# Kernel optimization log

Measured on AMD Instinct MI355X. Metric: run time of the kernel, lower is better.

Reference implementation:

```python
import jax, jax.numpy as jnp
import numpy as np

EPS = 1e-7
KERNELS = ((5, 5), (7, 1), (1, 7))
SCALES = (60, 30, 15, 8)


def avg_pool(x, kh, kw):
    # PyTorch AvgPool2d(kernel, stride=1, padding=(kh//2, kw//2)), count_include_pad=True
    s = jax.lax.reduce_window(x, 0.0, jax.lax.add, (1, 1, kh, kw), (1, 1, 1, 1),
                              ((0, 0), (0, 0), (kh // 2, kh // 2), (kw // 2, kw // 2)))
    return s / (kh * kw)


def resize_bilinear(x, oh, ow):
    # F.interpolate(mode='bilinear', align_corners=True), NCHW
    B, C, H, W = x.shape
    def coords(o, s):
        pos = jnp.arange(o) * ((s - 1) / max(o - 1, 1))
        i0 = jnp.floor(pos).astype(jnp.int32)
        i1 = jnp.minimum(i0 + 1, s - 1)
        w = (pos - i0).astype(x.dtype)
        return w, i0, i1
    wy, y0, y1 = coords(oh, H)
    wx, x0, x1 = coords(ow, W)
    rows = x[:, :, y0, :] * (1 - wy)[None, None, :, None] + x[:, :, y1, :] * wy[None, None, :, None]
    return rows[:, :, :, x0] * (1 - wx) + rows[:, :, :, x1] * wx


def setup_inputs() -> dict:
    key = jax.random.key(0)
    ks = jax.random.split(key, 12)
    B, C, H, shot = 2, 1024, 60, 1
    hid, tdim = 256, 300
    return {
        "weight": jax.random.uniform(ks[0], (B, shot, 1, 1), dtype=jnp.float32),
        "query_feat_4": jax.random.normal(ks[1], (B, C, H, H), dtype=jnp.float32),
        "supp_feats": jax.random.normal(ks[2], (shot, B, C, H, H), dtype=jnp.float32),
        "masks": jax.random.uniform(ks[3], (shot, B, 1, 473, 473), dtype=jnp.float32),
        "k": jax.random.normal(ks[4], (B, hid, H, H), dtype=jnp.float32),
        "text": jax.random.normal(ks[5], (B, tdim), dtype=jnp.float32),
        "prototype": jax.random.normal(ks[6], (B, hid, 1, 1), dtype=jnp.float32),
        "w_q": jax.random.normal(ks[7], (tdim + hid, hid), dtype=jnp.float32) * 0.05,
        "w_k": jax.random.normal(ks[8], (hid, hid), dtype=jnp.float32) * 0.05,
        "w_bl": jax.random.normal(ks[9], (hid, hid), dtype=jnp.float32) * 0.05,
        "w_proj": jax.random.normal(ks[10], (hid, hid), dtype=jnp.float32) * 0.05,
        "b_proj": jnp.zeros((hid,), dtype=jnp.float32),
    }


def reference(weight, query_feat_4, supp_feats, masks, k, text, prototype, w_q, w_k, w_bl, w_proj, b_proj):
    # ---------------- SPM: self-activation prior mask ----------------
    B, C, H, W = query_feat_4.shape
    S = H * W
    # pooled query features per kernel (shared across supports)
    q_pooled = []
    for (kh, kw) in KERNELS:
        tq = avg_pool(query_feat_4, kh, kw).reshape(B, C, S)
        tq_t = jnp.transpose(tq, (0, 2, 1))                    # [B,S,C]
        qn = jnp.sqrt((tq_t ** 2).sum(-1, keepdims=True))      # [B,S,1]
        q_pooled.append((tq_t, qn))

    corr_list = []
    for i in range(supp_feats.shape[0]):  # loop over shot (small, fixed)
        tmp_mask = resize_bilinear(masks[i], H, W)
        s = supp_feats[i] * tmp_mask
        region = []
        for (kh, kw), (tq_t, qn) in zip(KERNELS, q_pooled):
            ts = avg_pool(s, kh, kw).reshape(B, C, S)          # [B,C,S]
            sn = jnp.sqrt((ts ** 2).sum(1, keepdims=True))     # [B,1,S]
            sim = jnp.matmul(tq_t, ts) / (jnp.matmul(qn, sn) + EPS) * qn  # [B,S,S]
            sim = sim.mean(2)                                  # [B,S]
            mn = sim.min(1, keepdims=True)
            mx = sim.max(1, keepdims=True)
            sim = (sim - mn) / (mx - mn + EPS)
            region.append(sim.reshape(B, H, W))
        corr_list.append(jnp.stack(region, 1).mean(1))         # [B,H,W]
    corr = jnp.stack(corr_list, 1)                             # [B,shot,H,W]
    corr1 = (weight * corr).sum(1, keepdims=True)              # [B,1,H,W]
    corr2 = resize_bilinear(corr1, SCALES[1], SCALES[1])
    corr3 = resize_bilinear(corr1, SCALES[2], SCALES[2])
    corr4 = resize_bilinear(corr1, SCALES[3], SCALES[3])

    # ---------------- APA: bi-linear cross-modal attention ----------------
    Bk, hid, h, w = k.shape
    proto = prototype.reshape(Bk, 1, hid)                      # [B,1,hid]
    q = jnp.concatenate([text[:, None, :], proto], axis=-1)    # [B,1,embed]
    kx = jnp.einsum('oi,bihw->bohw', w_k, k).reshape(Bk, hid, h * w)
    kx = jnp.transpose(kx, (0, 2, 1))                          # [B,S,hid]
    qx = jnp.einsum('bqe,eh->bqh', q, w_q)                     # [B,1,hid]
    qw = jnp.einsum('bqh,hd->bqd', qx, w_bl)                   # bi_linear score
    score = jnp.einsum('bqd,bsd->bqs', qw, kx)                 # [B,1,S]
    score = jax.nn.softmax(score, axis=-1)
    out = jnp.einsum('bqs,bsd->bqd', score, kx)
    out = jnp.einsum('bqd,do->bqo', out, w_proj) + b_proj      # proj (dropout=eval no-op)
    out = out + proto
    return corr1, corr2, corr3, corr4, out
```

## Files before the change

kernel.cpp:

```cpp
#include <hip/hip_runtime.h>
#include <math.h>

#define EPSF 1e-7f
#define Bsz 2
#define Cch 1024
#define Hh 60
#define Ssz 3600
#define HID 256
#define TDIM 300
#define MH 473

#define TROWS 15
#define LROWS 21
#define LPITCH 68
#define CPG 8

#define OFF_SN2   7200
#define OFF_DOT   28800
#define OFF_ACC   50400
#define OFF_SCORE 57600
#define OFF_WMAP  64800
#define OFF_V     86400
#define OFF_U     92544
#define OFF_KBAR  93056
#define ZERO_OFF  OFF_SN2
#define ZERO_CNT  (OFF_WMAP - OFF_SN2)

__global__ void __launch_bounds__(256) k_pool_sn2(const float* __restrict__ supp,
                                                  const float* __restrict__ masks,
                                                  float* __restrict__ sn2g) {
    __shared__ float  mk[LROWS * LPITCH];
    __shared__ float2 raw[LROWS * LPITCH];
    __shared__ float2 h5s[LROWS * LPITCH];
    __shared__ float2 h7s[LROWS * LPITCH];
    int tid = threadIdx.x;
    int tile = blockIdx.x;
    int cg = blockIdx.y;
    int b = blockIdx.z;
    int y0 = tile * TROWS;

    const float2 z2 = {0.f, 0.f};
    for (int i = tid; i < LROWS * LPITCH; i += 256) {
        mk[i] = 0.f; raw[i] = z2; h5s[i] = z2; h7s[i] = z2;
    }
    __syncthreads();

    int lr[5], lx[5]; bool lv[5], la[5];
    #pragma unroll
    for (int j = 0; j < 5; ++j) {
        int idx = tid + 256 * j;
        int r = idx / 60, x = idx - 60 * r;
        lr[j] = r; lx[j] = x;
        la[j] = idx < 1260;
        int iy = y0 - 3 + r;
        lv[j] = la[j] && (iy >= 0) && (iy < Hh);
    }
    #pragma unroll
    for (int j = 0; j < 5; ++j)
        if (lv[j]) {
            int iy = y0 - 3 + lr[j];
            mk[lr[j] * LPITCH + 4 + lx[j]] =
                masks[(size_t)b * MH * MH + (size_t)(iy * 8) * MH + lx[j] * 8];
        }

    int orow[4], ox[4]; bool ov[4];
    #pragma unroll
    for (int j = 0; j < 4; ++j) {
        int o = tid + 256 * j;
        int oy = o / 60, x = o - 60 * oy;
        orow[j] = oy + 3; ox[j] = x; ov[j] = o < 900;
    }
    float a0[4] = {0,0,0,0}, a1[4] = {0,0,0,0}, a2[4] = {0,0,0,0};

    const float* chbase = supp + ((size_t)b * Cch + (size_t)cg * CPG) * Ssz + (y0 - 3) * 60;
    float pf0[5], pf1[5];
    #pragma unroll
    for (int j = 0; j < 5; ++j) {
        pf0[j] = lv[j] ? chbase[tid + 256 * j] : 0.f;
        pf1[j] = lv[j] ? chbase[Ssz + tid + 256 * j] : 0.f;
    }

    for (int p = 0; p < CPG / 2; ++p) {
        __syncthreads();
        #pragma unroll
        for (int j = 0; j < 5; ++j)
            if (lv[j]) {
                float m = mk[lr[j] * LPITCH + 4 + lx[j]];
                raw[lr[j] * LPITCH + 4 + lx[j]] = make_float2(pf0[j] * m, pf1[j] * m);
            }
        __syncthreads();
        #pragma unroll
        for (int j = 0; j < 5; ++j)
            if (la[j]) {
                int base = lr[j] * LPITCH + 4 + lx[j];
                float2 m3 = raw[base - 3], m2 = raw[base - 2], m1 = raw[base - 1];
                float2 c0 = raw[base], p1 = raw[base + 1], p2 = raw[base + 2], p3 = raw[base + 3];
                float2 h5, h7;
                h5.x = m2.x + m1.x + c0.x + p1.x + p2.x;
                h5.y = m2.y + m1.y + c0.y + p1.y + p2.y;
                h7.x = h5.x + m3.x + p3.x;
                h7.y = h5.y + m3.y + p3.y;
                h5s[base] = h5; h7s[base] = h7;
            }
        __syncthreads();
        if (p + 1 < CPG / 2) {
            const float* nb = chbase + (size_t)(2 * p + 2) * Ssz;
            #pragma unroll
            for (int j = 0; j < 5; ++j) {
                pf0[j] = lv[j] ? nb[tid + 256 * j] : 0.f;
                pf1[j] = lv[j] ? nb[Ssz + tid + 256 * j] : 0.f;
            }
        }
        #pragma unroll
        for (int j = 0; j < 4; ++j)
            if (ov[j]) {
                int base = orow[j] * LPITCH + 4 + ox[j];
                float2 sa = h5s[base - 2*LPITCH], sb = h5s[base - LPITCH], sc0 = h5s[base];
                float2 sd = h5s[base + LPITCH], se = h5s[base + 2*LPITCH];
                float p55x = (sa.x + sb.x + sc0.x + sd.x + se.x) * (1.f / 25.f);
                float p55y = (sa.y + sb.y + sc0.y + sd.y + se.y) * (1.f / 25.f);
                float2 ra = raw[base - 3*LPITCH], rb = raw[base - 2*LPITCH], rc = raw[base - LPITCH];
                float2 rd = raw[base], re = raw[base + LPITCH], rf = raw[base + 2*LPITCH], rg = raw[base + 3*LPITCH];
                float p71x = (ra.x + rb.x + rc.x + rd.x + re.x + rf.x + rg.x) * (1.f / 7.f);
                float p71y = (ra.y + rb.y + rc.y + rd.y + re.y + rf.y + rg.y) * (1.f / 7.f);
                float2 h7v = h7s[base];
                float p17x = h7v.x * (1.f / 7.f), p17y = h7v.y * (1.f / 7.f);
                a0[j] += p55x * p55x + p55y * p55y;
                a1[j] += p71x * p71x + p71y * p71y;
                a2[j] += p17x * p17x + p17y * p17y;
            }
    }
    float* g0 = sn2g + ((size_t)b * 3 + 0) * Ssz;
    float* g1 = sn2g + ((size_t)b * 3 + 1) * Ssz;
    float* g2 = sn2g + ((size_t)b * 3 + 2) * Ssz;
    #pragma unroll
    for (int j = 0; j < 4; ++j)
        if (ov[j]) {
            int q = (y0 + orow[j] - 3) * 60 + ox[j];
            atomicAdd(&g0[q], a0[j]);
            atomicAdd(&g1[q], a1[j]);
            atomicAdd(&g2[q], a2[j]);
        }
}

__global__ void k_wmap(const float* __restrict__ sn2g, float* __restrict__ wmapg) {
    __shared__ float inv[LROWS * LPITCH];
    int tile = blockIdx.x;
    int bk = blockIdx.y;
    int kt = bk % 3;
    int tid = threadIdx.x;
    int y0 = tile * TROWS;
    for (int i = tid; i < LROWS * LPITCH; i += 256) inv[i] = 0.f;
    __syncthreads();
    const float* sn2 = sn2g + (size_t)bk * Ssz;
    #pragma unroll
    for (int j = 0; j < 5; ++j) {
        int idx = tid + 256 * j;
        if (idx < 1260) {
            int r = idx / 60, x = idx - 60 * r;
            int iy = y0 - 3 + r;
            if (iy >= 0 && iy < Hh)
                inv[r * LPITCH + 4 + x] = 1.0f / sqrtf(fmaxf(sn2[iy * 60 + x], 1e-30f));
        }
    }
    __syncthreads();
    int kh = (kt == 0) ? 5 : (kt == 1) ? 7 : 1;
    int kw = (kt == 0) ? 5 : (kt == 2) ? 7 : 1;
    int rh = kh / 2, rw = kw / 2;
    float norm = 1.f / (float)(kh * kw);
    #pragma unroll
    for (int j = 0; j < 4; ++j) {
        int o = tid + 256 * j;
        if (o < 900) {
            int oy = o / 60, x = o - 60 * oy;
            int base = (oy + 3) * LPITCH + 4 + x;
            float s = 0.f;
            for (int dy = -rh; dy <= rh; ++dy)
                for (int dx = -rw; dx <= rw; ++dx)
                    s += inv[base + dy * LPITCH + dx];
            wmapg[(size_t)bk * Ssz + (y0 + oy) * 60 + x] = s * norm;
        }
    }
}

__global__ void k_v(const float* __restrict__ supp, const float* __restrict__ masks,
                    float* __restrict__ ws) {
    int c = blockIdx.x, b = blockIdx.y;
    int tid = threadIdx.x;
    const float* sp = supp + ((size_t)b * Cch + c) * Ssz;
    const float* mbase = masks + (size_t)b * MH * MH;
    const float* w0 = ws + OFF_WMAP + (size_t)(b * 3 + 0) * Ssz;
    const float* w1 = ws + OFF_WMAP + (size_t)(b * 3 + 1) * Ssz;
    const float* w2 = ws + OFF_WMAP + (size_t)(b * 3 + 2) * Ssz;
    float a0 = 0, a1 = 0, a2 = 0;
    for (int q = tid; q < Ssz; q += 256) {
        int y = q / Hh, x = q - y * Hh;
        float s = sp[q] * mbase[(size_t)(y * 8) * MH + x * 8];
        a0 += s * w0[q]; a1 += s * w1[q]; a2 += s * w2[q];
    }
    __shared__ float red[3][256];
    red[0][tid] = a0; red[1][tid] = a1; red[2][tid] = a2;
    __syncthreads();
    for (int off = 128; off > 0; off >>= 1) {
        if (tid < off) {
            red[0][tid] += red[0][tid + off];
            red[1][tid] += red[1][tid + off];
            red[2][tid] += red[2][tid + off];
        }
        __syncthreads();
    }
    if (tid == 0) {
        ws[OFF_V + (size_t)(b * 3 + 0) * Cch + c] = red[0][0];
        ws[OFF_V + (size_t)(b * 3 + 1) * Cch + c] = red[1][0];
        ws[OFF_V + (size_t)(b * 3 + 2) * Cch + c] = red[2][0];
    }
}

__global__ void k_dot(const float* __restrict__ query, float* __restrict__ ws) {
    int qt = blockIdx.x, cc = blockIdx.y, b = blockIdx.z;
    int q = qt * 256 + threadIdx.x;
    if (q >= Ssz) return;
    const float* v0 = ws + OFF_V + (size_t)(b * 3 + 0) * Cch;
    const float* v1 = ws + OFF_V + (size_t)(b * 3 + 1) * Cch;
    const float* v2 = ws + OFF_V + (size_t)(b * 3 + 2) * Cch;
    float a0 = 0, a1 = 0, a2 = 0;
    int c0 = cc * 64;
    for (int c = c0; c < c0 + 64; ++c) {
        float qv = query[((size_t)b * Cch + c) * Ssz + q];
        a0 += qv * v0[c]; a1 += qv * v1[c]; a2 += qv * v2[c];
    }
    atomicAdd(&ws[OFF_DOT + (size_t)(b * 3 + 0) * Ssz + q], a0);
    atomicAdd(&ws[OFF_DOT + (size_t)(b * 3 + 1) * Ssz + q], a1);
    atomicAdd(&ws[OFF_DOT + (size_t)(b * 3 + 2) * Ssz + q], a2);
}

__global__ void k_sim(float* __restrict__ ws) {
    __shared__ float dpad[66 * LPITCH];
    __shared__ float h5p[66 * LPITCH];
    __shared__ float h7p[66 * LPITCH];
    __shared__ float red[256];
    int bk = blockIdx.x; int b = bk / 3; int kt = bk % 3;
    int tid = threadIdx.x;
    const float* dg = ws + OFF_DOT + (size_t)bk * Ssz;
    for (int i = tid; i < 66 * LPITCH; i += 256) {
        int r = i / LPITCH, col = i - r * LPITCH;
        int y = r - 3, x = col - 4;
        dpad[i] = (y >= 0 && y < Hh && x >= 0 && x < Hh) ? dg[y * Hh + x] : 0.f;
    }
    __syncthreads();
    for (int idx = tid; idx < 66 * 60; idx += 256) {
        int r = idx / 60, x = idx - 60 * r;
        int base = r * LPITCH + 4 + x;
        float m3 = dpad[base - 3], m2 = dpad[base - 2], m1 = dpad[base - 1];
        float c0 = dpad[base], p1 = dpad[base + 1], p2 = dpad[base + 2], p3 = dpad[base + 3];
        float h5 = m2 + m1 + c0 + p1 + p2;
        h5p[base] = h5;
        h7p[base] = h5 + m3 + p3;
    }
    __syncthreads();
    float norm = ((kt == 0) ? (1.f / 25.f) : (1.f / 7.f)) * (1.f / (float)Ssz);
    float vals[15];
    float vmin = INFINITY, vmax = -INFINITY;
    #pragma unroll
    for (int j = 0; j < 15; ++j) {
        int q = tid + j * 256;
        if (q < Ssz) {
            int y = q / Hh, x = q - y * Hh;
            int base = (y + 3) * LPITCH + 4 + x;
            float s;
            if (kt == 0)
                s = h5p[base - 2*LPITCH] + h5p[base - LPITCH] + h5p[base]
                  + h5p[base + LPITCH] + h5p[base + 2*LPITCH];
            else if (kt == 1)
                s = dpad[base - 3*LPITCH] + dpad[base - 2*LPITCH] + dpad[base - LPITCH]
                  + dpad[base] + dpad[base + LPITCH] + dpad[base + 2*LPITCH] + dpad[base + 3*LPITCH];
            else
                s = h7p[base];
            float val = s * norm;
            vals[j] = val;
            vmin = fminf(vmin, val); vmax = fmaxf(vmax, val);
        }
    }
    red[tid] = vmin; __syncthreads();
    for (int off = 128; off > 0; off >>= 1) {
        if (tid < off) red[tid] = fminf(red[tid], red[tid + off]);
        __syncthreads();
    }
    float mn = red[0]; __syncthreads();
    red[tid] = vmax; __syncthreads();
    for (int off = 128; off > 0; off >>= 1) {
        if (tid < off) red[tid] = fmaxf(red[tid], red[tid + off]);
        __syncthreads();
    }
    float mx = red[0];
    float inv = 1.f / (mx - mn + EPSF);
    #pragma unroll
    for (int j = 0; j < 15; ++j) {
        int q = tid + j * 256;
        if (q < Ssz) atomicAdd(&ws[OFF_ACC + (size_t)b * Ssz + q], (vals[j] - mn) * inv);
    }
}

__global__ void k_final(const float* __restrict__ weight, const float* __restrict__ ws,
                        float* __restrict__ out) {
    int idx = blockIdx.x * 256 + threadIdx.x;
    if (idx < Bsz * Ssz) {
        int b = idx / Ssz, q = idx - b * Ssz;
        out[idx] = weight[b] * (1.f / 3.f) * ws[OFF_ACC + (size_t)b * Ssz + q];
        return;
    }
    int r = idx - Bsz * Ssz;
    int O, outbase;
    if (r < 1800)       { O = 30; outbase = 7200; }
    else if (r < 2250)  { O = 15; outbase = 9000; r -= 1800; }
    else if (r < 2378)  { O = 8;  outbase = 9450; r -= 2250; }
    else return;
    int n = O * O;
    int b = r / n, p = r - b * n;
    int y = p / O, x = p - y * O;
    float sc = (float)(Hh - 1) / (float)(O - 1);
    float py = y * sc, px = x * sc;
    int y0 = (int)floorf(py), x0 = (int)floorf(px);
    int y1 = min(y0 + 1, Hh - 1), x1 = min(x0 + 1, Hh - 1);
    float wy = py - y0, wx = px - x0;
    const float* src = ws + OFF_ACC + (size_t)b * Ssz;
    float v = src[y0 * Hh + x0] * (1.f - wy) * (1.f - wx)
            + src[y1 * Hh + x0] * wy * (1.f - wx)
            + src[y0 * Hh + x1] * (1.f - wy) * wx
            + src[y1 * Hh + x1] * wy * wx;
    out[outbase + r] = v * weight[b] * (1.f / 3.f);
}

__global__ void __launch_bounds__(1024, 1)
k_apa_u(const float* __restrict__ text, const float* __restrict__ proto,
        const float* __restrict__ w_q, const float* __restrict__ w_bl,
        const float* __restrict__ w_k, float* __restrict__ ws) {
    int b = blockIdx.x;
    int tid = threadIdx.x;
    int lane = tid & 63, w = tid >> 6;
    __shared__ float4 p4[16][64];
    __shared__ float qxs[256], qws[256];
    const float4* wq4 = (const float4*)w_q;
    const float4* wbl4 = (const float4*)w_bl;
    const float4* wk4 = (const float4*)w_k;

    float4 acc = {0.f, 0.f, 0.f, 0.f};
    #pragma unroll
    for (int j = 0; j < 35; ++j) {
        int e = w + 16 * j;
        if (e < TDIM + HID) {
            float x = (e < TDIM) ? text[b * TDIM + e] : proto[b * HID + e - TDIM];
            float4 f = wq4[(size_t)e * 64 + lane];
            acc.x += x * f.x; acc.y += x * f.y; acc.z += x * f.z; acc.w += x * f.w;
        }
    }
    p4[w][lane] = acc;
    __syncthreads();
    if (tid < 256) {
        const float* pf = (const float*)p4;
        float s = 0.f;
        #pragma unroll
        for (int ww = 0; ww < 16; ++ww) s += pf[ww * 256 + tid];
        qxs[tid] = s;
    }
    __syncthreads();

    acc.x = acc.y = acc.z = acc.w = 0.f;
    #pragma unroll
    for (int j = 0; j < 16; ++j) {
        int e = w + 16 * j;
        float x = qxs[e];
        float4 f = wbl4[(size_t)e * 64 + lane];
        acc.x += x * f.x; acc.y += x * f.y; acc.z += x * f.z; acc.w += x * f.w;
    }
    p4[w][lane] = acc;
    __syncthreads();
    if (tid < 256) {
        const float* pf = (const float*)p4;
        float s = 0.f;
        #pragma unroll
        for (int ww = 0; ww < 16; ++ww) s += pf[ww * 256 + tid];
        qws[tid] = s;
    }
    __syncthreads();

    acc.x = acc.y = acc.z = acc.w = 0.f;
    #pragma unroll
    for (int j = 0; j < 16; ++j) {
        int e = w + 16 * j;
        float x = qws[e];
        float4 f = wk4[(size_t)e * 64 + lane];
        acc.x += x * f.x; acc.y += x * f.y; acc.z += x * f.z; acc.w += x * f.w;
    }
    p4[w][lane] = acc;
    __syncthreads();
    if (tid < 256) {
        const float* pf = (const float*)p4;
        float s = 0.f;
        #pragma unroll
        for (int ww = 0; ww < 16; ++ww) s += pf[ww * 256 + tid];
        ws[OFF_U + b * HID + tid] = s;
    }
}

__global__ void k_score(const float* __restrict__ kin, float* __restrict__ ws) {
    int st = blockIdx.x, ic = blockIdx.y, b = blockIdx.z;
    int s = st * 256 + threadIdx.x;
    if (s >= Ssz) return;
    const float* u = ws + OFF_U + b * HID;
    float acc = 0.f;
    int i0 = ic * 64;
    for (int i = i0; i < i0 + 64; ++i)
        acc += u[i] * kin[((size_t)b * HID + i) * Ssz + s];
    atomicAdd(&ws[OFF_SCORE + (size_t)b * Ssz + s], acc);
}

__global__ void k_softmax(float* __restrict__ ws) {
    int b = blockIdx.x; int tid = threadIdx.x;
    __shared__ float red[256];
    float* sc = ws + OFF_SCORE + (size_t)b * Ssz;
    float vals[15];
    float mx = -INFINITY;
    for (int j = 0; j < 15; ++j) {
        int s = tid + j * 256;
        if (s < Ssz) { vals[j] = sc[s]; mx = fmaxf(mx, vals[j]); }
    }
    red[tid] = mx; __syncthreads();
    for (int off = 128; off > 0; off >>= 1) {
        if (tid < off) red[tid] = fmaxf(red[tid], red[tid + off]);
        __syncthreads();
    }
    mx = red[0]; __syncthreads();
    float sum = 0.f;
    for (int j = 0; j < 15; ++j) {
        int s = tid + j * 256;
        if (s < Ssz) { vals[j] = expf(vals[j] - mx); sum += vals[j]; }
    }
    red[tid] = sum; __syncthreads();
    for (int off = 128; off > 0; off >>= 1) {
        if (tid < off) red[tid] += red[tid + off];
        __syncthreads();
    }
    float inv = 1.f / red[0];
    for (int j = 0; j < 15; ++j) {
        int s = tid + j * 256;
        if (s < Ssz) sc[s] = vals[j] * inv;
    }
}

__global__ void k_kbar(const float* __restrict__ kin, float* __restrict__ ws) {
    int i = blockIdx.x, b = blockIdx.y;
    int tid = threadIdx.x;
    const float* p = ws + OFF_SCORE + (size_t)b * Ssz;
    const float* kr = kin + ((size_t)b * HID + i) * Ssz;
    float acc = 0.f;
    for (int s = tid; s < Ssz; s += 256) acc += p[s] * kr[s];
    __shared__ float red[256];
    red[tid] = acc; __syncthreads();
    for (int off = 128; off > 0; off >>= 1) {
        if (tid < off) red[tid] += red[tid + off];
        __syncthreads();
    }
    if (tid == 0) ws[OFF_KBAR + b * HID + i] = red[0];
}

__global__ void __launch_bounds__(1024, 1)
k_apa_out(const float* __restrict__ w_k, const float* __restrict__ w_proj,
          const float* __restrict__ b_proj, const float* __restrict__ proto,
          const float* __restrict__ ws, float* __restrict__ out) {
    int b = blockIdx.x;
    int tid = threadIdx.x;
    int lane = tid & 63, w = tid >> 6;
    __shared__ float4 kbs[64];
    __shared__ float o1s[256];
    __shared__ float4 p4[16][64];
    const float4* wk4 = (const float4*)w_k;
    const float4* wp4 = (const float4*)w_proj;

    if (tid < 64) kbs[tid] = ((const float4*)(ws + OFF_KBAR + b * HID))[tid];
    __syncthreads();

    float4 kb4 = kbs[lane];
    #pragma unroll
    for (int r = 0; r < 16; ++r) {
        int h = w + 16 * r;
        float4 f = wk4[(size_t)h * 64 + lane];
        float p = f.x * kb4.x + f.y * kb4.y + f.z * kb4.z + f.w * kb4.w;
        #pragma unroll
        for (int m = 32; m >= 1; m >>= 1) p += __shfl_xor(p, m, 64);
        if (lane == 0) o1s[h] = p;
    }
    __syncthreads();

    float4 acc = {0.f, 0.f, 0.f, 0.f};
    #pragma unroll
    for (int j = 0; j < 16; ++j) {
        int d = w + 16 * j;
        float x = o1s[d];
        float4 f = wp4[(size_t)d * 64 + lane];
        acc.x += x * f.x; acc.y += x * f.y; acc.z += x * f.z; acc.w += x * f.w;
    }
    p4[w][lane] = acc;
    __syncthreads();
    if (tid < 256) {
        const float* pf = (const float*)p4;
        float s = 0.f;
        #pragma unroll
        for (int ww = 0; ww < 16; ++ww) s += pf[ww * 256 + tid];
        out[9578 + b * HID + tid] = s + b_proj[tid] + proto[b * HID + tid];
    }
}

extern "C" void kernel_launch(void* const* d_in, const int* in_sizes, int n_in,
                              void* d_out, int out_size, void* d_ws, size_t ws_size,
                              hipStream_t stream) {
    const float* weight = (const float*)d_in[0];
    const float* query  = (const float*)d_in[1];
    const float* supp   = (const float*)d_in[2];
    const float* masks  = (const float*)d_in[3];
    const float* kin    = (const float*)d_in[4];
    const float* text   = (const float*)d_in[5];
    const float* proto  = (const float*)d_in[6];
    const float* w_q    = (const float*)d_in[7];
    const float* w_k    = (const float*)d_in[8];
    const float* w_bl   = (const float*)d_in[9];
    const float* w_proj = (const float*)d_in[10];
    const float* b_proj = (const float*)d_in[11];
    float* out = (float*)d_out;
    float* ws  = (float*)d_ws;

    hipMemsetAsync(ws + ZERO_OFF, 0, (size_t)ZERO_CNT * sizeof(float), stream);

    k_pool_sn2<<<dim3(4, Cch / CPG, Bsz), 256, 0, stream>>>(supp, masks, ws + OFF_SN2);
    k_wmap<<<dim3(4, 6), 256, 0, stream>>>(ws + OFF_SN2, ws + OFF_WMAP);
    k_v<<<dim3(Cch, Bsz), 256, 0, stream>>>(supp, masks, ws);
    k_dot<<<dim3(15, Cch / 64, Bsz), 256, 0, stream>>>(query, ws);
    k_sim<<<6, 256, 0, stream>>>(ws);
    k_final<<<(Bsz * Ssz + 2378 + 255) / 256, 256, 0, stream>>>(weight, ws, out);

    k_apa_u<<<Bsz, 1024, 0, stream>>>(text, proto, w_q, w_bl, w_k, ws);
    k_score<<<dim3(15, 4, Bsz), 256, 0, stream>>>(kin, ws);
    k_softmax<<<Bsz, 256, 0, stream>>>(ws);
    k_kbar<<<dim3(HID, Bsz), 256, 0, stream>>>(kin, ws);
    k_apa_out<<<Bsz, 1024, 0, stream>>>(w_k, w_proj, b_proj, proto, ws, out);
}
```

Before: 232.1 us.

## Fuse sim/final and softmax/kbar, fold mask into wmap, replace atomics with partials

Several kernels are merged: the final normalisation and bilinear resize move into k_sim, and the softmax is folded into k_kbar, which recomputes max and sum per block from partial scores. The mask multiply moves into k_wmap so k_v becomes a float4 dot product with wave-shuffle reductions. Atomic accumulation in k_dot and k_score is replaced by per-group partial buffers summed by the consumer, and the memset becomes a zeroing kernel that also clears the output. The intent is fewer launches, fewer atomics and less reduction overhead. In exchange k_kbar redoes the softmax reduction in each of its 512 blocks and k_sim runs on only 6 blocks.

```diff
diff --git a/kernel.cpp b/kernel.cpp
--- a/kernel.cpp
+++ b/kernel.cpp
@@ -15,16 +15,21 @@
 #define LPITCH 68
 #define CPG 8
 
-#define OFF_SN2   7200
-#define OFF_DOT   28800
-#define OFF_ACC   50400
-#define OFF_SCORE 57600
-#define OFF_WMAP  64800
-#define OFF_V     86400
-#define OFF_U     92544
-#define OFF_KBAR  93056
-#define ZERO_OFF  OFF_SN2
-#define ZERO_CNT  (OFF_WMAP - OFF_SN2)
+#define OFF_SN2    0
+#define OFF_WMAP   21600
+#define OFF_V      43200
+#define OFF_U      49344
+#define OFF_KBAR   49856
+#define OFF_DOTP   50368
+#define OFF_SCOREP 395968
+#define ZERO_WS    21600
+#define ZERO_OUT   9578
+
+__global__ void k_zero(float* __restrict__ ws, float* __restrict__ out) {
+    int i = blockIdx.x * 256 + threadIdx.x;
+    if (i < ZERO_WS) ws[i] = 0.f;
+    else if (i < ZERO_WS + ZERO_OUT) out[i - ZERO_WS] = 0.f;
+}
 
 __global__ void __launch_bounds__(256) k_pool_sn2(const float* __restrict__ supp,
                                                   const float* __restrict__ masks,
@@ -143,11 +148,12 @@
         }
 }
 
-__global__ void k_wmap(const float* __restrict__ sn2g, float* __restrict__ wmapg) {
+__global__ void k_wmap(const float* __restrict__ sn2g, const float* __restrict__ masks,
+                       float* __restrict__ wmapg) {
     __shared__ float inv[LROWS * LPITCH];
     int tile = blockIdx.x;
     int bk = blockIdx.y;
-    int kt = bk % 3;
+    int b = bk / 3, kt = bk % 3;
     int tid = threadIdx.x;
     int y0 = tile * TROWS;
     for (int i = tid; i < LROWS * LPITCH; i += 256) inv[i] = 0.f;
@@ -178,41 +184,45 @@
             for (int dy = -rh; dy <= rh; ++dy)
                 for (int dx = -rw; dx <= rw; ++dx)
                     s += inv[base + dy * LPITCH + dx];
-            wmapg[(size_t)bk * Ssz + (y0 + oy) * 60 + x] = s * norm;
-        }
-    }
-}
-
-__global__ void k_v(const float* __restrict__ supp, const float* __restrict__ masks,
-                    float* __restrict__ ws) {
+            int gy = y0 + oy;
+            float m = masks[(size_t)b * MH * MH + (size_t)(gy * 8) * MH + x * 8];
+            wmapg[(size_t)bk * Ssz + gy * 60 + x] = s * norm * m;
+        }
+    }
+}
+
+__global__ void k_v(const float* __restrict__ supp, float* __restrict__ ws) {
     int c = blockIdx.x, b = blockIdx.y;
     int tid = threadIdx.x;
-    const float* sp = supp + ((size_t)b * Cch + c) * Ssz;
-    const float* mbase = masks + (size_t)b * MH * MH;
-    const float* w0 = ws + OFF_WMAP + (size_t)(b * 3 + 0) * Ssz;
-    const float* w1 = ws + OFF_WMAP + (size_t)(b * 3 + 1) * Ssz;
-    const float* w2 = ws + OFF_WMAP + (size_t)(b * 3 + 2) * Ssz;
+    int lane = tid & 63, w = tid >> 6;
+    const float4* sp4 = (const float4*)(supp + ((size_t)b * Cch + c) * Ssz);
+    const float4* w04 = (const float4*)(ws + OFF_WMAP + (size_t)(b * 3 + 0) * Ssz);
+    const float4* w14 = (const float4*)(ws + OFF_WMAP + (size_t)(b * 3 + 1) * Ssz);
+    const float4* w24 = (const float4*)(ws + OFF_WMAP + (size_t)(b * 3 + 2) * Ssz);
     float a0 = 0, a1 = 0, a2 = 0;
-    for (int q = tid; q < Ssz; q += 256) {
-        int y = q / Hh, x = q - y * Hh;
-        float s = sp[q] * mbase[(size_t)(y * 8) * MH + x * 8];
-        a0 += s * w0[q]; a1 += s * w1[q]; a2 += s * w2[q];
-    }
-    __shared__ float red[3][256];
-    red[0][tid] = a0; red[1][tid] = a1; red[2][tid] = a2;
-    __syncthreads();
-    for (int off = 128; off > 0; off >>= 1) {
-        if (tid < off) {
-            red[0][tid] += red[0][tid + off];
-            red[1][tid] += red[1][tid + off];
-            red[2][tid] += red[2][tid + off];
-        }
-        __syncthreads();
-    }
-    if (tid == 0) {
-        ws[OFF_V + (size_t)(b * 3 + 0) * Cch + c] = red[0][0];
-        ws[OFF_V + (size_t)(b * 3 + 1) * Cch + c] = red[1][0];
-        ws[OFF_V + (size_t)(b * 3 + 2) * Cch + c] = red[2][0];
+    #pragma unroll
+    for (int j = 0; j < 4; ++j) {
+        int idx = tid + 256 * j;
+        if (idx < 900) {
+            float4 f = sp4[idx];
+            float4 g0 = w04[idx], g1 = w14[idx], g2 = w24[idx];
+            a0 += f.x * g0.x + f.y * g0.y + f.z * g0.z + f.w * g0.w;
+            a1 += f.x * g1.x + f.y * g1.y + f.z * g1.z + f.w * g1.w;
+            a2 += f.x * g2.x + f.y * g2.y + f.z * g2.z + f.w * g2.w;
+        }
+    }
+    #pragma unroll
+    for (int m = 32; m >= 1; m >>= 1) {
+        a0 += __shfl_xor(a0, m, 64);
+        a1 += __shfl_xor(a1, m, 64);
+        a2 += __shfl_xor(a2, m, 64);
+    }
+    __shared__ float r[3][4];
+    if (lane == 0) { r[0][w] = a0; r[1][w] = a1; r[2][w] = a2; }
+    __syncthreads();
+    if (tid < 3) {
+        float s = r[tid][0] + r[tid][1] + r[tid][2] + r[tid][3];
+        ws[OFF_V + (size_t)(b * 3 + tid) * Cch + c] = s;
     }
 }
 
@@ -225,110 +235,120 @@
     const float* v2 = ws + OFF_V + (size_t)(b * 3 + 2) * Cch;
     float a0 = 0, a1 = 0, a2 = 0;
     int c0 = cc * 64;
+    #pragma unroll 8
     for (int c = c0; c < c0 + 64; ++c) {
         float qv = query[((size_t)b * Cch + c) * Ssz + q];
         a0 += qv * v0[c]; a1 += qv * v1[c]; a2 += qv * v2[c];
     }
-    atomicAdd(&ws[OFF_DOT + (size_t)(b * 3 + 0) * Ssz + q], a0);
-    atomicAdd(&ws[OFF_DOT + (size_t)(b * 3 + 1) * Ssz + q], a1);
-    atomicAdd(&ws[OFF_DOT + (size_t)(b * 3 + 2) * Ssz + q], a2);
-}
-
-__global__ void k_sim(float* __restrict__ ws) {
+    float* dst = ws + OFF_DOTP + (size_t)((cc * 2 + b) * 3) * Ssz + q;
+    dst[0] = a0; dst[Ssz] = a1; dst[2 * Ssz] = a2;
+}
+
+__global__ void __launch_bounds__(1024) k_sim(const float* __restrict__ weight,
+                                              float* __restrict__ ws,
+                                              float* __restrict__ out) {
     __shared__ float dpad[66 * LPITCH];
-    __shared__ float h5p[66 * LPITCH];
-    __shared__ float h7p[66 * LPITCH];
-    __shared__ float red[256];
+    __shared__ float hbuf[66 * LPITCH];
+    __shared__ float rmin[16], rmax[16];
     int bk = blockIdx.x; int b = bk / 3; int kt = bk % 3;
     int tid = threadIdx.x;
-    const float* dg = ws + OFF_DOT + (size_t)bk * Ssz;
-    for (int i = tid; i < 66 * LPITCH; i += 256) {
+    int lane = tid & 63, w = tid >> 6;
+
+    const float* dp0 = ws + OFF_DOTP + (size_t)(b * 3 + kt) * Ssz;
+    for (int i = tid; i < 66 * LPITCH; i += 1024) {
         int r = i / LPITCH, col = i - r * LPITCH;
         int y = r - 3, x = col - 4;
-        dpad[i] = (y >= 0 && y < Hh && x >= 0 && x < Hh) ? dg[y * Hh + x] : 0.f;
-    }
-    __syncthreads();
-    for (int idx = tid; idx < 66 * 60; idx += 256) {
-        int r = idx / 60, x = idx - 60 * r;
-        int base = r * LPITCH + 4 + x;
-        float m3 = dpad[base - 3], m2 = dpad[base - 2], m1 = dpad[base - 1];
-        float c0 = dpad[base], p1 = dpad[base + 1], p2 = dpad[base + 2], p3 = dpad[base + 3];
-        float h5 = m2 + m1 + c0 + p1 + p2;
-        h5p[base] = h5;
-        h7p[base] = h5 + m3 + p3;
+        float s = 0.f;
+        if (y >= 0 && y < Hh && x >= 0 && x < Hh) {
+            int q = y * Hh + x;
+            #pragma unroll
+            for (int g = 0; g < 16; ++g) s += dp0[(size_t)g * 6 * Ssz + q];
+        }
+        dpad[i] = s;
+    }
+    __syncthreads();
+    if (kt != 1) {
+        for (int idx = tid; idx < 66 * 60; idx += 1024) {
+            int r = idx / 60, x = idx - 60 * r;
+            int base = r * LPITCH + 4 + x;
+            if (kt == 0) {
+                hbuf[base] = dpad[base - 2] + dpad[base - 1] + dpad[base]
+                           + dpad[base + 1] + dpad[base + 2];
+            } else {
+                hbuf[base] = dpad[base - 3] + dpad[base - 2] + dpad[base - 1] + dpad[base]
+                           + dpad[base + 1] + dpad[base + 2] + dpad[base + 3];
+            }
+        }
     }
     __syncthreads();
     float norm = ((kt == 0) ? (1.f / 25.f) : (1.f / 7.f)) * (1.f / (float)Ssz);
-    float vals[15];
+    float vals[4];
     float vmin = INFINITY, vmax = -INFINITY;
     #pragma unroll
-    for (int j = 0; j < 15; ++j) {
-        int q = tid + j * 256;
+    for (int j = 0; j < 4; ++j) {
+        int q = tid + j * 1024;
         if (q < Ssz) {
             int y = q / Hh, x = q - y * Hh;
             int base = (y + 3) * LPITCH + 4 + x;
             float s;
             if (kt == 0)
-                s = h5p[base - 2*LPITCH] + h5p[base - LPITCH] + h5p[base]
-                  + h5p[base + LPITCH] + h5p[base + 2*LPITCH];
+                s = hbuf[base - 2*LPITCH] + hbuf[base - LPITCH] + hbuf[base]
+                  + hbuf[base + LPITCH] + hbuf[base + 2*LPITCH];
             else if (kt == 1)
                 s = dpad[base - 3*LPITCH] + dpad[base - 2*LPITCH] + dpad[base - LPITCH]
                   + dpad[base] + dpad[base + LPITCH] + dpad[base + 2*LPITCH] + dpad[base + 3*LPITCH];
             else
-                s = h7p[base];
+                s = hbuf[base];
             float val = s * norm;
             vals[j] = val;
             vmin = fminf(vmin, val); vmax = fmaxf(vmax, val);
         }
     }
-    red[tid] = vmin; __syncthreads();
-    for (int off = 128; off > 0; off >>= 1) {
-        if (tid < off) red[tid] = fminf(red[tid], red[tid + off]);
-        __syncthreads();
-    }
-    float mn = red[0]; __syncthreads();
-    red[tid] = vmax; __syncthreads();
-    for (int off = 128; off > 0; off >>= 1) {
-        if (tid < off) red[tid] = fmaxf(red[tid], red[tid + off]);
-        __syncthreads();
-    }
-    float mx = red[0];
+    #pragma unroll
+    for (int m = 32; m >= 1; m >>= 1) {
+        vmin = fminf(vmin, __shfl_xor(vmin, m, 64));
+        vmax = fmaxf(vmax, __shfl_xor(vmax, m, 64));
+    }
+    if (lane == 0) { rmin[w] = vmin; rmax[w] = vmax; }
+    __syncthreads();
+    float mn = rmin[0], mx = rmax[0];
+    #pragma unroll
+    for (int ww = 1; ww < 16; ++ww) {
+        mn = fminf(mn, rmin[ww]); mx = fmaxf(mx, rmax[ww]);
+    }
     float inv = 1.f / (mx - mn + EPSF);
-    #pragma unroll
-    for (int j = 0; j < 15; ++j) {
-        int q = tid + j * 256;
-        if (q < Ssz) atomicAdd(&ws[OFF_ACC + (size_t)b * Ssz + q], (vals[j] - mn) * inv);
-    }
-}
-
-__global__ void k_final(const float* __restrict__ weight, const float* __restrict__ ws,
-                        float* __restrict__ out) {
-    int idx = blockIdx.x * 256 + threadIdx.x;
-    if (idx < Bsz * Ssz) {
-        int b = idx / Ssz, q = idx - b * Ssz;
-        out[idx] = weight[b] * (1.f / 3.f) * ws[OFF_ACC + (size_t)b * Ssz + q];
-        return;
-    }
-    int r = idx - Bsz * Ssz;
-    int O, outbase;
-    if (r < 1800)       { O = 30; outbase = 7200; }
-    else if (r < 2250)  { O = 15; outbase = 9000; r -= 1800; }
-    else if (r < 2378)  { O = 8;  outbase = 9450; r -= 2250; }
-    else return;
-    int n = O * O;
-    int b = r / n, p = r - b * n;
-    int y = p / O, x = p - y * O;
-    float sc = (float)(Hh - 1) / (float)(O - 1);
-    float py = y * sc, px = x * sc;
-    int y0 = (int)floorf(py), x0 = (int)floorf(px);
-    int y1 = min(y0 + 1, Hh - 1), x1 = min(x0 + 1, Hh - 1);
-    float wy = py - y0, wx = px - x0;
-    const float* src = ws + OFF_ACC + (size_t)b * Ssz;
-    float v = src[y0 * Hh + x0] * (1.f - wy) * (1.f - wx)
-            + src[y1 * Hh + x0] * wy * (1.f - wx)
-            + src[y0 * Hh + x1] * (1.f - wy) * wx
-            + src[y1 * Hh + x1] * wy * wx;
-    out[outbase + r] = v * weight[b] * (1.f / 3.f);
+    float wq3 = weight[b] * (1.f / 3.f);
+    __syncthreads();
+    #pragma unroll
+    for (int j = 0; j < 4; ++j) {
+        int q = tid + j * 1024;
+        if (q < Ssz) {
+            float vn = (vals[j] - mn) * inv;
+            atomicAdd(&out[b * Ssz + q], wq3 * vn);
+            hbuf[q] = vn;
+        }
+    }
+    __syncthreads();
+    #pragma unroll
+    for (int j = 0; j < 2; ++j) {
+        int o = tid + j * 1024;
+        if (o >= 1189) continue;
+        int O, p, outi;
+        if (o < 900)       { O = 30; p = o;        outi = 7200 + b * 900 + p; }
+        else if (o < 1125) { O = 15; p = o - 900;  outi = 9000 + b * 225 + p; }
+        else               { O = 8;  p = o - 1125; outi = 9450 + b * 64 + p; }
+        int y = p / O, x = p - y * O;
+        float sc = 59.f / (float)(O - 1);
+        float py = y * sc, px = x * sc;
+        int y0 = (int)floorf(py), x0 = (int)floorf(px);
+        int y1 = min(y0 + 1, 59), x1 = min(x0 + 1, 59);
+        float wy = py - y0, wx = px - x0;
+        float v = hbuf[y0 * 60 + x0] * (1.f - wy) * (1.f - wx)
+                + hbuf[y1 * 60 + x0] * wy * (1.f - wx)
+                + hbuf[y0 * 60 + x1] * (1.f - wy) * wx
+                + hbuf[y1 * 60 + x1] * wy * wx;
+        atomicAdd(&out[outi], wq3 * v);
+    }
 }
 
 __global__ void __launch_bounds__(1024, 1)
@@ -404,64 +424,76 @@
 }
 
 __global__ void k_score(const float* __restrict__ kin, float* __restrict__ ws) {
-    int st = blockIdx.x, ic = blockIdx.y, b = blockIdx.z;
+    int st = blockIdx.x, g = blockIdx.y, b = blockIdx.z;
     int s = st * 256 + threadIdx.x;
     if (s >= Ssz) return;
     const float* u = ws + OFF_U + b * HID;
     float acc = 0.f;
-    int i0 = ic * 64;
+    int i0 = g * 64;
+    #pragma unroll 8
     for (int i = i0; i < i0 + 64; ++i)
         acc += u[i] * kin[((size_t)b * HID + i) * Ssz + s];
-    atomicAdd(&ws[OFF_SCORE + (size_t)b * Ssz + s], acc);
-}
-
-__global__ void k_softmax(float* __restrict__ ws) {
-    int b = blockIdx.x; int tid = threadIdx.x;
-    __shared__ float red[256];
-    float* sc = ws + OFF_SCORE + (size_t)b * Ssz;
-    float vals[15];
-    float mx = -INFINITY;
-    for (int j = 0; j < 15; ++j) {
-        int s = tid + j * 256;
-        if (s < Ssz) { vals[j] = sc[s]; mx = fmaxf(mx, vals[j]); }
-    }
-    red[tid] = mx; __syncthreads();
-    for (int off = 128; off > 0; off >>= 1) {
-        if (tid < off) red[tid] = fmaxf(red[tid], red[tid + off]);
-        __syncthreads();
-    }
-    mx = red[0]; __syncthreads();
-    float sum = 0.f;
-    for (int j = 0; j < 15; ++j) {
-        int s = tid + j * 256;
-        if (s < Ssz) { vals[j] = expf(vals[j] - mx); sum += vals[j]; }
-    }
-    red[tid] = sum; __syncthreads();
-    for (int off = 128; off > 0; off >>= 1) {
-        if (tid < off) red[tid] += red[tid + off];
-        __syncthreads();
-    }
-    float inv = 1.f / red[0];
-    for (int j = 0; j < 15; ++j) {
-        int s = tid + j * 256;
-        if (s < Ssz) sc[s] = vals[j] * inv;
-    }
+    ws[OFF_SCOREP + (size_t)(g * 2 + b) * Ssz + s] = acc;
 }
 
 __global__ void k_kbar(const float* __restrict__ kin, float* __restrict__ ws) {
     int i = blockIdx.x, b = blockIdx.y;
     int tid = threadIdx.x;
-    const float* p = ws + OFF_SCORE + (size_t)b * Ssz;
-    const float* kr = kin + ((size_t)b * HID + i) * Ssz;
-    float acc = 0.f;
-    for (int s = tid; s < Ssz; s += 256) acc += p[s] * kr[s];
-    __shared__ float red[256];
-    red[tid] = acc; __syncthreads();
-    for (int off = 128; off > 0; off >>= 1) {
-        if (tid < off) red[tid] += red[tid + off];
-        __syncthreads();
-    }
-    if (tid == 0) ws[OFF_KBAR + b * HID + i] = red[0];
+    int lane = tid & 63, w = tid >> 6;
+    __shared__ float r1[4], r2[4];
+    const float4* s0 = (const float4*)(ws + OFF_SCOREP + (size_t)(0 * 2 + b) * Ssz);
+    const float4* s1 = (const float4*)(ws + OFF_SCOREP + (size_t)(1 * 2 + b) * Ssz);
+    const float4* s2 = (const float4*)(ws + OFF_SCOREP + (size_t)(2 * 2 + b) * Ssz);
+    const float4* s3 = (const float4*)(ws + OFF_SCOREP + (size_t)(3 * 2 + b) * Ssz);
+    float4 sv[4]; bool act[4];
+    float mx = -INFINITY;
+    #pragma unroll
+    for (int j = 0; j < 4; ++j) {
+        int idx = tid + 256 * j;
+        act[j] = idx < 900;
+        if (act[j]) {
+            float4 a = s0[idx], c = s1[idx], d = s2[idx], e = s3[idx];
+            float4 v;
+            v.x = a.x + c.x + d.x + e.x;
+            v.y = a.y + c.y + d.y + e.y;
+            v.z = a.z + c.z + d.z + e.z;
+            v.w = a.w + c.w + d.w + e.w;
+            sv[j] = v;
+            mx = fmaxf(mx, fmaxf(fmaxf(v.x, v.y), fmaxf(v.z, v.w)));
+        }
+    }
+    #pragma unroll
+    for (int m = 32; m >= 1; m >>= 1) mx = fmaxf(mx, __shfl_xor(mx, m, 64));
+    if (lane == 0) r1[w] = mx;
+    __syncthreads();
+    mx = fmaxf(fmaxf(r1[0], r1[1]), fmaxf(r1[2], r1[3]));
+    __syncthreads();
+    const float4* kr = (const float4*)(kin + ((size_t)b * HID + i) * Ssz);
+    float se = 0.f, wsum = 0.f;
+    #pragma unroll
+    for (int j = 0; j < 4; ++j) {
+        if (act[j]) {
+            int idx = tid + 256 * j;
+            float4 v = sv[j];
+            float ex = expf(v.x - mx), ey = expf(v.y - mx);
+            float ez = expf(v.z - mx), ew = expf(v.w - mx);
+            se += ex + ey + ez + ew;
+            float4 k4 = kr[idx];
+            wsum += ex * k4.x + ey * k4.y + ez * k4.z + ew * k4.w;
+        }
+    }
+    #pragma unroll
+    for (int m = 32; m >= 1; m >>= 1) {
+        se += __shfl_xor(se, m, 64);
+        wsum += __shfl_xor(wsum, m, 64);
+    }
+    if (lane == 0) { r1[w] = se; r2[w] = wsum; }
+    __syncthreads();
+    if (tid == 0) {
+        float seT = r1[0] + r1[1] + r1[2] + r1[3];
+        float wsT = r2[0] + r2[1] + r2[2] + r2[3];
+        ws[OFF_KBAR + b * HID + i] = wsT / seT;
+    }
 }
 
 __global__ void __launch_bounds__(1024, 1)
@@ -529,18 +561,16 @@
     float* out = (float*)d_out;
     float* ws  = (float*)d_ws;
 
-    hipMemsetAsync(ws + ZERO_OFF, 0, (size_t)ZERO_CNT * sizeof(float), stream);
+    k_zero<<<(ZERO_WS + ZERO_OUT + 255) / 256, 256, 0, stream>>>(ws, out);
 
     k_pool_sn2<<<dim3(4, Cch / CPG, Bsz), 256, 0, stream>>>(supp, masks, ws + OFF_SN2);
-    k_wmap<<<dim3(4, 6), 256, 0, stream>>>(ws + OFF_SN2, ws + OFF_WMAP);
-    k_v<<<dim3(Cch, Bsz), 256, 0, stream>>>(supp, masks, ws);
-    k_dot<<<dim3(15, Cch / 64, Bsz), 256, 0, stream>>>(query, ws);
-    k_sim<<<6, 256, 0, stream>>>(ws);
-    k_final<<<(Bsz * Ssz + 2378 + 255) / 256, 256, 0, stream>>>(weight, ws, out);
+    k_wmap<<<dim3(4, 6), 256, 0, stream>>>(ws + OFF_SN2, masks, ws + OFF_WMAP);
+    k_v<<<dim3(Cch, Bsz), 256, 0, stream>>>(supp, ws);
+    k_dot<<<dim3(15, 16, Bsz), 256, 0, stream>>>(query, ws);
+    k_sim<<<6, 1024, 0, stream>>>(weight, ws, out);
 
     k_apa_u<<<Bsz, 1024, 0, stream>>>(text, proto, w_q, w_bl, w_k, ws);
     k_score<<<dim3(15, 4, Bsz), 256, 0, stream>>>(kin, ws);
-    k_softmax<<<Bsz, 256, 0, stream>>>(ws);
     k_kbar<<<dim3(HID, Bsz), 256, 0, stream>>>(kin, ws);
     k_apa_out<<<Bsz, 1024, 0, stream>>>(w_k, w_proj, b_proj, proto, ws, out);
 }
```

Result: faster. 209.5 us (-9.7%).
